# Kernel optimization log

Measured on AMD Instinct MI355X. Metric: run time of the kernel, lower is better.

Reference implementation:

```python
import jax, jax.numpy as jnp
import numpy as np

N = 200_000   # nodes
E = 6_400_000 # edges (avg degree 32)
F_IN = 32     # num_node_features
G = 64        # graphs in batch
K = 3         # TAGConv hops (PyG default)
N_CLS = 13


def _lin_params(key, cin, cout, stack):
    kw, kb = jax.random.split(key)
    s = 1.0 / np.sqrt(cin)
    W = jax.random.uniform(kw, (stack, cin, cout), jnp.float32, -s, s)
    b = jax.random.uniform(kb, (stack, cout), jnp.float32, -s, s)
    return W, b


def setup_inputs():
    key = jax.random.key(0)
    ks = jax.random.split(key, 8)
    x = jax.random.normal(ks[0], (N, F_IN), dtype=jnp.float32)
    edge_index = jax.random.randint(ks[1], (2, E), 0, N)
    batch = jnp.sort(jax.random.randint(ks[2], (N,), 0, G))
    W1, b1 = _lin_params(ks[3], F_IN, 16, K + 1)
    W2, b2 = _lin_params(ks[4], 16, 32, K + 1)
    W3, b3 = _lin_params(ks[5], 32, 16, K + 1)
    Wfc, bfc = _lin_params(ks[6], 16, N_CLS, 1)
    return {"x": x, "edge_index": edge_index, "batch": batch,
            "W1": W1, "b1": b1, "W2": W2, "b2": b2, "W3": W3, "b3": b3,
            "Wfc": Wfc[0], "bfc": bfc[0]}


def _gcn_norm(row, col, n):
    # PyG gcn_norm with add_self_loops=False, edge_weight=1:
    # deg[i] = in-degree at target nodes; norm_e = d^{-1/2}[row] * d^{-1/2}[col]
    deg = jax.ops.segment_sum(jnp.ones(row.shape[0], jnp.float32), col, num_segments=n)
    dinv = jnp.where(deg > 0, jax.lax.rsqrt(jnp.maximum(deg, 1.0)), 0.0)
    return dinv[row] * dinv[col]


def _tagconv(x, row, col, norm, W, b):
    # out = sum_k A_norm^k x @ W[k] + b[k]
    out = x @ W[0] + b[0]
    h = x
    for k in range(1, W.shape[0]):
        msg = h[row] * norm[:, None]                       # [E, C] gather
        h = jax.ops.segment_sum(msg, col, num_segments=x.shape[0])  # scatter-add
        out = out + h @ W[k] + b[k]
    return out


def reference(x, edge_index, batch, W1, b1, W2, b2, W3, b3, Wfc, bfc):
    row, col = edge_index[0], edge_index[1]
    norm = _gcn_norm(row, col, x.shape[0])
    h = jax.nn.relu(_tagconv(x, row, col, norm, W1, b1))
    h = jax.nn.relu(_tagconv(h, row, col, norm, W2, b2))
    h = jax.nn.relu(_tagconv(h, row, col, norm, W3, b3))
    # global_mean_pool over graph ids
    summed = jax.ops.segment_sum(h, batch, num_segments=G)
    cnt = jax.ops.segment_sum(jnp.ones(h.shape[0], h.dtype), batch, num_segments=G)
    pooled = summed / jnp.maximum(cnt, 1.0)[:, None]
    logits = pooled @ Wfc + bfc
    return jax.nn.log_softmax(logits, axis=1)
```

## Files before the change

kernel.cpp:

```cpp
#include <hip/hip_runtime.h>
#include <hip/hip_fp16.h>

#define F_INPUT 32
#define NGRAPH 64
#define NCLS 13

#define NBUCK 128
#define DPB 1563
#define CAP 53760
#define PART_CHUNK 12800
#define NFINE 16
#define DPB_F 98
#define CAP_F 3584
#define SPLIT2 4

static inline int cdiv(int a, int b){ return (a + b - 1) / b; }

typedef float floatx2 __attribute__((ext_vector_type(2)));

__device__ inline uint2 pack4h(float s0, float s1, float s2, float s3){
  __half2 a = __floats2half2_rn(s0, s1);
  __half2 b = __floats2half2_rn(s2, s3);
  uint2 r;
  r.x = *(unsigned int*)&a;
  r.y = *(unsigned int*)&b;
  return r;
}
__device__ inline void unpack4h(uint2 q, float& f0, float& f1, float& f2, float& f3){
  __half2 a = *(__half2*)&q.x;
  __half2 b = *(__half2*)&q.y;
  float2 fa = __half22float2(a), fb = __half22float2(b);
  f0 = fa.x; f1 = fa.y; f2 = fb.x; f3 = fb.y;
}

__device__ inline unsigned int pack4fp8(float f0, float f1, float f2, float f3){
  int r = 0;
  r = __builtin_amdgcn_cvt_pk_fp8_f32(f0, f1, r, false);
  r = __builtin_amdgcn_cvt_pk_fp8_f32(f2, f3, r, true);
  return (unsigned int)r;
}
__device__ inline void unpack4fp8v(unsigned int q, floatx2& lo, floatx2& hi){
  lo = __builtin_amdgcn_cvt_pk_f32_fp8((int)q, false);
  hi = __builtin_amdgcn_cvt_pk_f32_fp8((int)q, true);
}

__global__ __launch_bounds__(1024)
void k_part(const int* __restrict__ row, const int* __restrict__ col,
            int* __restrict__ gcur, int* __restrict__ packed, int E, int nbuck){
  __shared__ int scol[PART_CHUNK];
  __shared__ int hist[NBUCK];
  __shared__ int gbase[NBUCK];
  __shared__ int cur[NBUCK];
  int t = threadIdx.x;
  if (t < NBUCK) hist[t] = 0;
  __syncthreads();
  int base = blockIdx.x * PART_CHUNK;
  int nloc = min(PART_CHUNK, E - base);
  for (int i = t; i < nloc; i += 1024){
    int c = col[base + i];
    scol[i] = c;
    atomicAdd(&hist[c / DPB], 1);
  }
  __syncthreads();
  if (t < nbuck){
    gbase[t] = atomicAdd(&gcur[t], hist[t]);
    cur[t] = 0;
  }
  __syncthreads();
  for (int i = t; i < nloc; i += 1024){
    int c = scol[i];
    int b = c / DPB;
    int j = gbase[b] + atomicAdd(&cur[b], 1);
    if (j < CAP){
      int src = row[base + i];
      packed[(size_t)b * CAP + j] = (src << 11) | (c - b * DPB);
    }
  }
}

__global__ __launch_bounds__(1024)
void k_part2(const int* __restrict__ gcur, const int* __restrict__ packed1,
             int* __restrict__ gcur2, int* __restrict__ packed2){
  __shared__ int hist[NFINE];
  __shared__ int gb[NFINE];
  __shared__ int cur[NFINE];
  int b = blockIdx.x >> 2;
  int s = blockIdx.x & 3;
  int t = threadIdx.x;
  int count = min(gcur[b], CAP);
  int seg = (count + SPLIT2 - 1) / SPLIT2;
  int lo = s * seg;
  int hi = min(lo + seg, count);
  if (t < NFINE) hist[t] = 0;
  __syncthreads();
  int ebase = b * CAP;
  for (int i = lo + t; i < hi; i += 1024)
    atomicAdd(&hist[(packed1[ebase + i] & 2047) / DPB_F], 1);
  __syncthreads();
  if (t < NFINE){
    gb[t] = atomicAdd(&gcur2[b * NFINE + t], hist[t]);
    cur[t] = 0;
  }
  __syncthreads();
  for (int i = lo + t; i < hi; i += 1024){
    int v = packed1[ebase + i];
    int ldst = v & 2047;
    int f = ldst / DPB_F;
    int j = gb[f] + atomicAdd(&cur[f], 1);
    if (j < CAP_F)
      packed2[(size_t)(b * NFINE + f) * CAP_F + j] = ((v >> 11) << 7) | (ldst - f * DPB_F);
  }
}

__global__ __launch_bounds__(512)
void k_bfill2(const int* __restrict__ gcur2, const int* __restrict__ packed2,
              int* __restrict__ csr, int2* __restrict__ offAB,
              float* __restrict__ dinv, int N){
  __shared__ int ein[CAP_F];
  __shared__ int eout[CAP_F];
  __shared__ int hist[128];
  __shared__ int scan[128];
  __shared__ int cur[128];
  int fb = blockIdx.x;
  int b = fb >> 4, f = fb & 15;
  int t = threadIdx.x;
  int count = min(gcur2[fb], CAP_F);
  size_t gbase = (size_t)fb * CAP_F;
  if (t < 128) hist[t] = 0;
  __syncthreads();
  for (int i = t; i < count; i += 512){
    int v = packed2[gbase + i];
    ein[i] = v;
    atomicAdd(&hist[v & 127], 1);
  }
  __syncthreads();
  if (t < 128){
    int ln = t & 63;
    int x = (t < DPB_F) ? hist[t] : 0;
    #pragma unroll
    for (int d = 1; d < 64; d <<= 1){
      int y = __shfl_up(x, d);
      if (ln >= d) x += y;
    }
    scan[t] = x;
  }
  __syncthreads();
  if (t >= 64 && t < 128) scan[t] += scan[63];
  __syncthreads();
  if (t < DPB_F){
    int deg = hist[t];
    int excl = scan[t] - deg;
    cur[t] = excl;
    int ld = f * DPB_F + t;
    int d = b * DPB + ld;
    if (ld < DPB && d < N){
      offAB[d] = make_int2((int)gbase + excl, (int)gbase + excl + deg);
      dinv[d] = deg > 0 ? rsqrtf((float)deg) : 0.f;
    }
  }
  __syncthreads();
  for (int i = t; i < count; i += 512){
    int v = ein[i];
    int pos = atomicAdd(&cur[v & 127], 1);
    eout[pos] = v >> 7;
  }
  __syncthreads();
  for (int i = t; i < count; i += 512)
    csr[gbase + i] = eout[i];
}

__global__ void k_xw4h(const float* __restrict__ X, const float* __restrict__ W,
                       const float* __restrict__ b, const float* __restrict__ dinv,
                       uint2* __restrict__ z0, uint2* __restrict__ z1,
                       uint2* __restrict__ z2, unsigned int* __restrict__ z3p8, int n){
  __shared__ float sW[2048];
  __shared__ float sb[16];
  for (int i = threadIdx.x; i < 2048; i += blockDim.x) sW[i] = W[i];
  if (threadIdx.x < 16)
    sb[threadIdx.x] = b[threadIdx.x] + b[16+threadIdx.x] + b[32+threadIdx.x] + b[48+threadIdx.x];
  __syncthreads();
  int v = blockIdx.x * blockDim.x + threadIdx.x;
  if (v >= n) return;
  float xr[32];
  const float4* xp = (const float4*)(X + (size_t)v * 32);
  #pragma unroll
  for (int j = 0; j < 8; j++){ float4 t = xp[j]; xr[4*j]=t.x; xr[4*j+1]=t.y; xr[4*j+2]=t.z; xr[4*j+3]=t.w; }
  float dv = dinv[v];
  #pragma unroll
  for (int k = 0; k < 4; k++){
    float o[16];
    #pragma unroll
    for (int c = 0; c < 16; c++) o[c] = 0.f;
    const float* wk = &sW[k * 512];
    #pragma unroll
    for (int i = 0; i < 32; i++){
      float xi = xr[i];
      #pragma unroll
      for (int c = 0; c < 16; c++) o[c] += xi * wk[i*16 + c];
    }
    if (k == 3){
      unsigned int* dp8 = z3p8 + (size_t)v * 4;
      #pragma unroll
      for (int j = 0; j < 4; j++)
        dp8[j] = pack4fp8(o[4*j]*dv, o[4*j+1]*dv, o[4*j+2]*dv, o[4*j+3]*dv);
    } else {
      uint2* dst;
      if (k == 0){
        #pragma unroll
        for (int c = 0; c < 16; c++) o[c] += sb[c];
        dst = z0;
      } else if (k == 1) dst = z1;
      else dst = z2;
      uint2* dp = dst + (size_t)v * 4;
      #pragma unroll
      for (int j = 0; j < 4; j++) dp[j] = pack4h(o[4*j], o[4*j+1], o[4*j+2], o[4*j+3]);
    }
  }
}

__global__ void k_prop8(const int2* __restrict__ offAB,
                        const int* __restrict__ csr,
                        const float* __restrict__ dinv,
                        const unsigned int* __restrict__ pin,
                        const uint2* __restrict__ addv,
                        uint2* __restrict__ hout,
                        unsigned int* __restrict__ pout,
                        int do_relu, int n){
  int gw = (int)((blockIdx.x * (size_t)blockDim.x + threadIdx.x) >> 6);
  int nw = (int)(((size_t)gridDim.x * blockDim.x) >> 6);
  int lane = threadIdx.x & 63;
  int g = lane >> 4;
  int cq = lane & 3;
  int esub = (lane >> 2) & 3;
  for (int vb = gw * 4; vb < n; vb += nw * 4){
    int v = min(vb + g, n - 1);
    int2 ab = offAB[v];
    float dv = dinv[v];
    floatx2 a01 = {0.f, 0.f}, a23 = {0.f, 0.f};
    int e = ab.x + esub;
    int e1 = ab.y;
    for (; e + 4 < e1; e += 8){
      int sa = csr[e];
      int sb = csr[e + 4];
      unsigned int qa = pin[(size_t)sa * 4 + cq];
      unsigned int qb = pin[(size_t)sb * 4 + cq];
      floatx2 la, ha, lb, hb;
      unpack4fp8v(qa, la, ha);
      unpack4fp8v(qb, lb, hb);
      a01 += la + lb;
      a23 += ha + hb;
    }
    if (e < e1){
      int s = csr[e];
      unsigned int q = pin[(size_t)s * 4 + cq];
      floatx2 l, h;
      unpack4fp8v(q, l, h);
      a01 += l;
      a23 += h;
    }
    float a0 = a01.x, a1 = a01.y, a2 = a23.x, a3 = a23.y;
    a0 += __shfl_xor(a0, 8); a1 += __shfl_xor(a1, 8); a2 += __shfl_xor(a2, 8); a3 += __shfl_xor(a3, 8);
    a0 += __shfl_xor(a0, 4); a1 += __shfl_xor(a1, 4); a2 += __shfl_xor(a2, 4); a3 += __shfl_xor(a3, 4);
    if (esub == 0 && vb + g < n){
      float s0 = dv * a0, s1 = dv * a1, s2 = dv * a2, s3 = dv * a3;
      if (addv){
        float g0, g1, g2, g3;
        unpack4h(addv[(size_t)v * 4 + cq], g0, g1, g2, g3);
        s0 += g0; s1 += g1; s2 += g2; s3 += g3;
      }
      if (do_relu){
        s0 = fmaxf(s0, 0.f); s1 = fmaxf(s1, 0.f); s2 = fmaxf(s2, 0.f); s3 = fmaxf(s3, 0.f);
      }
      if (hout) hout[(size_t)v * 4 + cq] = pack4h(s0, s1, s2, s3);
      if (pout) pout[(size_t)v * 4 + cq] = pack4fp8(dv * s0, dv * s1, dv * s2, dv * s3);
    }
  }
}

__global__ void k_lin4h(const uint2* __restrict__ g0, const uint2* __restrict__ g1,
                        const uint2* __restrict__ g2, const uint2* __restrict__ g3,
                        const float* __restrict__ W, const float* __restrict__ b,
                        float* __restrict__ h2, int n){
  __shared__ float sW[2048];
  __shared__ float sb[32];
  for (int i = threadIdx.x; i < 2048; i += blockDim.x) sW[i] = W[i];
  if (threadIdx.x < 32)
    sb[threadIdx.x] = b[threadIdx.x] + b[32+threadIdx.x] + b[64+threadIdx.x] + b[96+threadIdx.x];
  __syncthreads();
  int v = blockIdx.x * blockDim.x + threadIdx.x;
  if (v >= n) return;
  float o[32];
  #pragma unroll
  for (int c = 0; c < 32; c++) o[c] = sb[c];
  #pragma unroll
  for (int k = 0; k < 4; k++){
    const uint2* gk = (k==0) ? g0 : (k==1) ? g1 : (k==2) ? g2 : g3;
    const uint2* gp = gk + (size_t)v * 4;
    float gr[16];
    #pragma unroll
    for (int j = 0; j < 4; j++) unpack4h(gp[j], gr[4*j], gr[4*j+1], gr[4*j+2], gr[4*j+3]);
    const float* wk = &sW[k * 512];
    #pragma unroll
    for (int i = 0; i < 16; i++){
      float gi = gr[i];
      #pragma unroll
      for (int c = 0; c < 32; c++) o[c] += gi * wk[i*32 + c];
    }
  }
  float4* dp = (float4*)(h2 + (size_t)v * 32);
  #pragma unroll
  for (int j = 0; j < 8; j++)
    dp[j] = make_float4(fmaxf(o[4*j],0.f), fmaxf(o[4*j+1],0.f), fmaxf(o[4*j+2],0.f), fmaxf(o[4*j+3],0.f));
}

__global__ void k_poolh(const __half* __restrict__ h, const int* __restrict__ batch,
                        float* __restrict__ pooled, float* __restrict__ cnt, int n){
  __shared__ float sacc[NGRAPH * 16];
  __shared__ float scnt[NGRAPH];
  for (int i = threadIdx.x; i < NGRAPH*16; i += blockDim.x) sacc[i] = 0.f;
  if (threadIdx.x < NGRAPH) scnt[threadIdx.x] = 0.f;
  __syncthreads();
  int t = blockIdx.x * blockDim.x + threadIdx.x;
  int c = t & 15;
  int stride = (gridDim.x * blockDim.x) >> 4;
  for (int v = t >> 4; v < n; v += stride){
    int b = batch[v];
    atomicAdd(&sacc[b*16 + c], __half2float(h[(size_t)v*16 + c]));
    if (c == 0) atomicAdd(&scnt[b], 1.f);
  }
  __syncthreads();
  for (int i = threadIdx.x; i < NGRAPH*16; i += blockDim.x)
    if (sacc[i] != 0.f) atomicAdd(&pooled[i], sacc[i]);
  if (threadIdx.x < NGRAPH && scnt[threadIdx.x] != 0.f) atomicAdd(&cnt[threadIdx.x], scnt[threadIdx.x]);
}

__global__ void k_head(const float* __restrict__ pooled, const float* __restrict__ cnt,
                       const float* __restrict__ Wfc, const float* __restrict__ bfc,
                       float* __restrict__ out){
  int g = threadIdx.x;
  if (g >= NGRAPH) return;
  float cc = fmaxf(cnt[g], 1.f);
  float p[16];
  #pragma unroll
  for (int i = 0; i < 16; i++) p[i] = pooled[g*16 + i] / cc;
  float logits[NCLS];
  #pragma unroll
  for (int j = 0; j < NCLS; j++){
    float s = bfc[j];
    #pragma unroll
    for (int i = 0; i < 16; i++) s += p[i] * Wfc[i*NCLS + j];
    logits[j] = s;
  }
  float m = logits[0];
  #pragma unroll
  for (int j = 1; j < NCLS; j++) m = fmaxf(m, logits[j]);
  float l = 0.f;
  #pragma unroll
  for (int j = 0; j < NCLS; j++) l += expf(logits[j] - m);
  l = logf(l);
  #pragma unroll
  for (int j = 0; j < NCLS; j++) out[g*NCLS + j] = logits[j] - m - l;
}

extern "C" void kernel_launch(void* const* d_in, const int* in_sizes, int n_in,
                              void* d_out, int out_size, void* d_ws, size_t ws_size,
                              hipStream_t stream) {
  const float* x    = (const float*)d_in[0];
  const int*   ei   = (const int*)  d_in[1];
  const int*   batch= (const int*)  d_in[2];
  const float* W1   = (const float*)d_in[3];
  const float* b1   = (const float*)d_in[4];
  const float* W2   = (const float*)d_in[5];
  const float* b2   = (const float*)d_in[6];
  const float* W3   = (const float*)d_in[7];
  const float* b3   = (const float*)d_in[8];
  const float* Wfc  = (const float*)d_in[9];
  const float* bfc  = (const float*)d_in[10];
  float* out = (float*)d_out;

  const int N = in_sizes[0] / F_INPUT;
  const int E = in_sizes[1] / 2;
  const int* row = ei;
  const int* col = ei + E;
  const int nbuck = cdiv(N, DPB);
  const int nfine = NBUCK * NFINE;

  char* w = (char*)d_ws;
  auto alloc = [&](size_t bytes)->char*{
    char* p = w;
    w += (bytes + 255) & ~(size_t)255;
    return p;
  };
  int*   gcur    = (int*)  alloc((size_t)NBUCK * 4);
  int*   gcur2   = (int*)  alloc((size_t)nfine * 4);
  int*   csr     = (int*)  alloc((size_t)nfine * CAP_F * 4);
  int*   packed2 = (int*)  alloc((size_t)nfine * CAP_F * 4);
  int2*  offAB   = (int2*) alloc((size_t)N * 8);
  float* dinv    = (float*)alloc((size_t)N * 4);
  uint2* F0      = (uint2*)alloc((size_t)N * 16 * 2);
  uint2* F1      = (uint2*)alloc((size_t)N * 16 * 2);
  uint2* F2      = (uint2*)alloc((size_t)N * 16 * 2);
  uint2* F3      = (uint2*)alloc((size_t)N * 16 * 2);
  unsigned int* P0 = (unsigned int*)alloc((size_t)N * 16);
  unsigned int* P1 = (unsigned int*)alloc((size_t)N * 16);
  unsigned int* P2 = (unsigned int*)alloc((size_t)N * 16);
  float* H2      = (float*)alloc((size_t)N * 32 * 4);
  float* pooled  = (float*)alloc((size_t)(NGRAPH*16 + NGRAPH) * 4);
  float* cnt     = pooled + NGRAPH*16;
  int*   packed1 = (int*)F0;
  (void)ws_size; (void)n_in; (void)out_size;

  (void)hipMemsetAsync(gcur, 0, (size_t)NBUCK * 4, stream);
  (void)hipMemsetAsync(gcur2, 0, (size_t)nfine * 4, stream);
  k_part  <<<cdiv(E, PART_CHUNK), 1024, 0, stream>>>(row, col, gcur, packed1, E, nbuck);
  k_part2 <<<NBUCK * SPLIT2, 1024, 0, stream>>>(gcur, packed1, gcur2, packed2);
  k_bfill2<<<nfine, 512, 0, stream>>>(gcur2, packed2, csr, offAB, dinv, N);

  const int PROP_BLOCKS = 2048;

  k_xw4h<<<cdiv(N,256), 256, 0, stream>>>(x, W1, b1, dinv, F0, F1, F2, P0, N);
  k_prop8<<<PROP_BLOCKS, 256, 0, stream>>>(offAB, csr, dinv, P0, F2, nullptr, P1, 0, N);
  k_prop8<<<PROP_BLOCKS, 256, 0, stream>>>(offAB, csr, dinv, P1, F1, nullptr, P2, 0, N);
  k_prop8<<<PROP_BLOCKS, 256, 0, stream>>>(offAB, csr, dinv, P2, F0, F0, P0, 1, N);

  k_prop8<<<PROP_BLOCKS, 256, 0, stream>>>(offAB, csr, dinv, P0, nullptr, F1, P1, 0, N);
  k_prop8<<<PROP_BLOCKS, 256, 0, stream>>>(offAB, csr, dinv, P1, nullptr, F2, P2, 0, N);
  k_prop8<<<PROP_BLOCKS, 256, 0, stream>>>(offAB, csr, dinv, P2, nullptr, F3, nullptr, 0, N);
  k_lin4h<<<cdiv(N,256), 256, 0, stream>>>(F0, F1, F2, F3, W2, b2, H2, N);

  k_xw4h<<<cdiv(N,256), 256, 0, stream>>>(H2, W3, b3, dinv, F0, F1, F2, P0, N);
  k_prop8<<<PROP_BLOCKS, 256, 0, stream>>>(offAB, csr, dinv, P0, F2, nullptr, P1, 0, N);
  k_prop8<<<PROP_BLOCKS, 256, 0, stream>>>(offAB, csr, dinv, P1, F1, nullptr, P2, 0, N);
  k_prop8<<<PROP_BLOCKS, 256, 0, stream>>>(offAB, csr, dinv, P2, F0, F3, nullptr, 1, N);

  (void)hipMemsetAsync(pooled, 0, (size_t)(NGRAPH*16 + NGRAPH) * 4, stream);
  k_poolh<<<512, 256, 0, stream>>>((const __half*)F3, batch, pooled, cnt, N);
  k_head<<<1, 64, 0, stream>>>(pooled, cnt, Wfc, bfc, out);
}
```

Before: 579.1 us.

## Locally sort edges by bucket in shared memory before coalesced scatter in k_part

```diff
diff --git a/kernel.cpp b/kernel.cpp
--- a/kernel.cpp
+++ b/kernel.cpp
@@ -8,7 +8,7 @@
 #define NBUCK 128
 #define DPB 1563
 #define CAP 53760
-#define PART_CHUNK 12800
+#define PART_CHUNK 4096
 #define NFINE 16
 #define DPB_F 98
 #define CAP_F 3584
@@ -44,37 +44,64 @@
   hi = __builtin_amdgcn_cvt_pk_f32_fp8((int)q, true);
 }
 
-__global__ __launch_bounds__(1024)
+__global__ __launch_bounds__(512)
 void k_part(const int* __restrict__ row, const int* __restrict__ col,
-            int* __restrict__ gcur, int* __restrict__ packed, int E, int nbuck){
-  __shared__ int scol[PART_CHUNK];
+            int* __restrict__ gcur, int* __restrict__ packed, int E){
+  __shared__ int vals[PART_CHUNK];
+  __shared__ int sorted[PART_CHUNK];
+  __shared__ unsigned char keyb[PART_CHUNK];
+  __shared__ unsigned char keyb2[PART_CHUNK];
   __shared__ int hist[NBUCK];
+  __shared__ int beg[NBUCK];
   __shared__ int gbase[NBUCK];
-  __shared__ int cur[NBUCK];
+  __shared__ int scan[NBUCK];
   int t = threadIdx.x;
   if (t < NBUCK) hist[t] = 0;
   __syncthreads();
   int base = blockIdx.x * PART_CHUNK;
   int nloc = min(PART_CHUNK, E - base);
-  for (int i = t; i < nloc; i += 1024){
+  for (int i = t; i < nloc; i += 512){
     int c = col[base + i];
-    scol[i] = c;
-    atomicAdd(&hist[c / DPB], 1);
-  }
-  __syncthreads();
-  if (t < nbuck){
-    gbase[t] = atomicAdd(&gcur[t], hist[t]);
-    cur[t] = 0;
-  }
-  __syncthreads();
-  for (int i = t; i < nloc; i += 1024){
-    int c = scol[i];
+    int src = row[base + i];
     int b = c / DPB;
-    int j = gbase[b] + atomicAdd(&cur[b], 1);
-    if (j < CAP){
-      int src = row[base + i];
-      packed[(size_t)b * CAP + j] = (src << 11) | (c - b * DPB);
-    }
+    keyb[i] = (unsigned char)b;
+    vals[i] = (src << 11) | (c - b * DPB);
+    atomicAdd(&hist[b], 1);
+  }
+  __syncthreads();
+  if (t < 128){
+    int ln = t & 63;
+    int x = hist[t];
+    #pragma unroll
+    for (int d = 1; d < 64; d <<= 1){
+      int y = __shfl_up(x, d);
+      if (ln >= d) x += y;
+    }
+    scan[t] = x;
+  }
+  __syncthreads();
+  if (t >= 64 && t < 128) scan[t] += scan[63];
+  __syncthreads();
+  if (t < NBUCK){
+    int deg = hist[t];
+    int excl = scan[t] - deg;
+    beg[t] = excl;
+    gbase[t] = atomicAdd(&gcur[t], deg);
+    hist[t] = excl;
+  }
+  __syncthreads();
+  for (int i = t; i < nloc; i += 512){
+    unsigned char b = keyb[i];
+    int pos = atomicAdd(&hist[b], 1);
+    sorted[pos] = vals[i];
+    keyb2[pos] = b;
+  }
+  __syncthreads();
+  for (int i = t; i < nloc; i += 512){
+    int b = keyb2[i];
+    int j = gbase[b] + (i - beg[b]);
+    if (j < CAP)
+      packed[(size_t)b * CAP + j] = sorted[i];
   }
 }
 
@@ -382,7 +409,6 @@
   const int E = in_sizes[1] / 2;
   const int* row = ei;
   const int* col = ei + E;
-  const int nbuck = cdiv(N, DPB);
   const int nfine = NBUCK * NFINE;
 
   char* w = (char*)d_ws;
@@ -412,7 +438,7 @@
 
   (void)hipMemsetAsync(gcur, 0, (size_t)NBUCK * 4, stream);
   (void)hipMemsetAsync(gcur2, 0, (size_t)nfine * 4, stream);
-  k_part  <<<cdiv(E, PART_CHUNK), 1024, 0, stream>>>(row, col, gcur, packed1, E, nbuck);
+  k_part  <<<cdiv(E, PART_CHUNK), 512, 0, stream>>>(row, col, gcur, packed1, E);
   k_part2 <<<NBUCK * SPLIT2, 1024, 0, stream>>>(gcur, packed1, gcur2, packed2);
   k_bfill2<<<nfine, 512, 0, stream>>>(gcur2, packed2, csr, offAB, dinv, N);
 
```

Measured after the change: 579.9 us. Within noise of the previous version (+0.1%).
